# Performance work log

Measured on AMD Instinct MI355X. Metric: run time of the kernel, lower is better.

## Reference

```python
import jax, jax.numpy as jnp
import numpy as np
from jax import lax

B, L = 2, 1024
D_MODEL, D_STATE, EXPAND, D_CONV = 1024, 16, 2, 4
D_INNER = EXPAND * D_MODEL            # 2048
DT_RANK = (D_MODEL + 15) // 16        # 64


def setup_inputs() -> dict:
    key = jax.random.key(0)
    ks = jax.random.split(key, 8)
    g = lambda k, shape, s=0.02: jax.random.normal(k, shape, dtype=jnp.float32) * s
    # Mamba-style A init: A = -exp(A_log), A_log = log(1..d_state) per channel
    A_log = jnp.log(jnp.broadcast_to(
        jnp.arange(1, D_STATE + 1, dtype=jnp.float32), (D_INNER, D_STATE)))
    return {
        "x": jax.random.normal(ks[0], (B, L, D_MODEL), dtype=jnp.float32),
        "W_in": g(ks[1], (D_MODEL, 2 * D_INNER)),
        "conv_w": g(ks[2], (D_INNER, D_CONV), 0.1),
        "conv_b": jnp.zeros((D_INNER,), jnp.float32),
        "W_x": g(ks[3], (D_INNER, DT_RANK + 2 * D_STATE)),
        "W_dt": g(ks[4], (DT_RANK, D_INNER)),
        "b_dt": g(ks[5], (D_INNER,), 0.1),
        "A_log": A_log,
        "D_skip": jnp.ones((D_INNER,), jnp.float32),
        "W_out": g(ks[6], (D_INNER, D_MODEL)),
    }


def reference(x, W_in, conv_w, conv_b, W_x, W_dt, b_dt, A_log, D_skip, W_out):
    # in_proj -> (u, z): [B, L, D_INNER] each
    xz = x @ W_in
    u, z = xz[..., :D_INNER], xz[..., D_INNER:]

    # causal depthwise conv1d, kernel D_CONV (small fixed loop over taps)
    up = jnp.pad(u, ((0, 0), (D_CONV - 1, 0), (0, 0)))
    u = sum(up[:, k:k + L, :] * conv_w[:, k] for k in range(D_CONV)) + conv_b
    u = jax.nn.silu(u)

    # input-dependent dt, B, C
    x_dbl = u @ W_x                                    # [B, L, dt_rank + 2N]
    dt = x_dbl[..., :DT_RANK]
    Bm = x_dbl[..., DT_RANK:DT_RANK + D_STATE]         # [B, L, N]
    Cm = x_dbl[..., DT_RANK + D_STATE:]                # [B, L, N]
    delta = jax.nn.softplus(dt @ W_dt + b_dt)          # [B, L, D]

    A = -jnp.exp(A_log)                                # [D, N]
    deltaA = jnp.exp(jnp.einsum('bld,dn->bldn', delta, A))   # [B, L, D, N]
    dBu = (delta * u)[..., None] * Bm[:, :, None, :]          # [B, L, D, N]

    def step(h, inp):
        dA_t, dBu_t, c_t = inp                         # [B,D,N],[B,D,N],[B,N]
        h = dA_t * h + dBu_t
        y_t = jnp.einsum('bdn,bn->bd', h, c_t)
        return h, y_t

    h0 = jnp.zeros((B, D_INNER, D_STATE), x.dtype)
    _, ys = lax.scan(step, h0,
                     (deltaA.transpose(1, 0, 2, 3),
                      dBu.transpose(1, 0, 2, 3),
                      Cm.transpose(1, 0, 2)))
    y = ys.transpose(1, 0, 2) + u * D_skip             # [B, L, D_INNER]
    y = y * jax.nn.silu(z)                             # gated output
    return y @ W_out                                   # [B, L, D_MODEL]
```

## Files before the change

kernel.cpp:

```cpp
#include <hip/hip_runtime.h>


typedef unsigned short u16;
typedef unsigned int   u32;

#define B_SZ 2
#define L_SZ 1024
#define DM   1024
#define DI   2048
#define DS   16
#define DTR  64
#define NXD  96
#define NCHUNK 16
#define CL   64
#define KSPLIT 8
#define KC     256
#define OSPLIT 2

typedef __bf16 bf16x8 __attribute__((ext_vector_type(8)));
typedef float  f32x4  __attribute__((ext_vector_type(4)));

__device__ __forceinline__ u16 f2bf(float f) {
    u32 x = __float_as_uint(f);
    x += 0x7fffu + ((x >> 16) & 1u);
    return (u16)(x >> 16);
}
__device__ __forceinline__ float bf2f(u16 v) {
    return __uint_as_float(((u32)v) << 16);
}

__device__ __forceinline__ void gld_lds16(const u16* g, u16* l) {
    __builtin_amdgcn_global_load_lds(
        (const __attribute__((address_space(1))) u32*)g,
        (__attribute__((address_space(3))) u32*)l, 16, 0, 0);
}

__device__ __forceinline__ void wg_barrier() {
    __asm__ volatile("" ::: "memory");
    __builtin_amdgcn_s_barrier();
    __asm__ volatile("" ::: "memory");
}
#define WAIT_VM12() __builtin_amdgcn_s_waitcnt(0xF7C)
#define WAIT_VM8()  __builtin_amdgcn_s_waitcnt(0xF78)
#define WAIT_VM4()  __builtin_amdgcn_s_waitcnt(0xF74)
#define WAIT_VM0()  __builtin_amdgcn_s_waitcnt(0xF70)
#define WAIT_LGKM0() __builtin_amdgcn_s_waitcnt(0xC07F)

__global__ __launch_bounds__(256) void gemm128p(
    const u16* __restrict__ A, const u16* __restrict__ BT,
    float* __restrict__ Cf, u16* __restrict__ Cb,
    const float* __restrict__ bias,
    int M, int N, int K, int KCHUNK, int op)
{
    __shared__ u16 As[4][128 * 32];
    __shared__ u16 Bs[4][128 * 32];

    const int tid  = threadIdx.x;
    const int wave = tid >> 6;
    const int lane = tid & 63;
    const int q    = lane >> 4;
    const int r16  = lane & 15;
    const int wm   = (wave & 1) * 64;
    const int wn   = (wave >> 1) * 64;
    const int m0   = blockIdx.y * 128;
    const int n0   = blockIdx.x * 128;
    const int kb   = blockIdx.z * KCHUNK;

    const u16* gA0 = A  + (size_t)(m0 + (tid >> 2))      * K + (tid & 3) * 8;
    const u16* gA1 = A  + (size_t)(m0 + 64 + (tid >> 2)) * K + (tid & 3) * 8;
    const u16* gB0 = BT + (size_t)(n0 + (tid >> 2))      * K + (tid & 3) * 8;
    const u16* gB1 = BT + (size_t)(n0 + 64 + (tid >> 2)) * K + (tid & 3) * 8;

    const int niter = KCHUNK >> 5;

    const int pre = niter < 3 ? niter : 3;
    for (int p = 0; p < pre; ++p) {
        const int k0 = kb + p * 32;
        gld_lds16(gA0 + k0, &As[p][tid * 8]);
        gld_lds16(gA1 + k0, &As[p][2048 + tid * 8]);
        gld_lds16(gB0 + k0, &Bs[p][tid * 8]);
        gld_lds16(gB1 + k0, &Bs[p][2048 + tid * 8]);
    }

    f32x4 acc[4][4];
#pragma unroll
    for (int s = 0; s < 4; ++s)
#pragma unroll
        for (int j = 0; j < 4; ++j) acc[s][j] = (f32x4){0.f, 0.f, 0.f, 0.f};

    for (int it = 0; it < niter; ++it) {
        if (it + 3 < niter) {
            const int k0 = kb + (it + 3) * 32;
            const int bi = (it + 3) & 3;
            gld_lds16(gA0 + k0, &As[bi][tid * 8]);
            gld_lds16(gA1 + k0, &As[bi][2048 + tid * 8]);
            gld_lds16(gB0 + k0, &Bs[bi][tid * 8]);
            gld_lds16(gB1 + k0, &Bs[bi][2048 + tid * 8]);
            WAIT_VM12();
        } else if (it + 2 < niter) {
            WAIT_VM8();
        } else if (it + 1 < niter) {
            WAIT_VM4();
        } else {
            WAIT_VM0();
        }
        wg_barrier();

        const int cur = it & 3;
        bf16x8 af[4], bfr[4];
#pragma unroll
        for (int s = 0; s < 4; ++s)
            af[s] = *(const bf16x8*)(&As[cur][(wm + s * 16 + r16) * 32 + q * 8]);
#pragma unroll
        for (int j = 0; j < 4; ++j)
            bfr[j] = *(const bf16x8*)(&Bs[cur][(wn + j * 16 + r16) * 32 + q * 8]);
#pragma unroll
        for (int s = 0; s < 4; ++s)
#pragma unroll
            for (int j = 0; j < 4; ++j)
                acc[s][j] = __builtin_amdgcn_mfma_f32_16x16x32_bf16(
                    af[s], bfr[j], acc[s][j], 0, 0, 0);

        wg_barrier();
    }

#pragma unroll
    for (int s = 0; s < 4; ++s) {
        const int row0 = m0 + wm + s * 16 + q * 4;
#pragma unroll
        for (int j = 0; j < 4; ++j) {
            const int col = n0 + wn + j * 16 + r16;
            if (op == 0) {
                float* Cz = Cf + (size_t)blockIdx.z * M * N;
#pragma unroll
                for (int i = 0; i < 4; ++i)
                    Cz[(size_t)(row0 + i) * N + col] = acc[s][j][i];
            } else if (op == 1) {
                const float bv = bias[col];
#pragma unroll
                for (int i = 0; i < 4; ++i) {
                    float v = acc[s][j][i] + bv;
                    v = (v > 20.f) ? v : log1pf(__expf(v));
                    Cf[(size_t)(row0 + i) * N + col] = v;
                }
            } else {
#pragma unroll
                for (int i = 0; i < 4; ++i)
                    Cb[(size_t)(row0 + i) * N + col] = f2bf(acc[s][j][i]);
            }
        }
    }
}

__global__ __launch_bounds__(256) void reduce_out(
    const float* __restrict__ part, float* __restrict__ out, int n)
{
    const int i = (blockIdx.x * 256 + threadIdx.x) * 4;
    if (i >= n) return;
    f32x4 v = *(const f32x4*)(part + i);
#pragma unroll
    for (int s = 1; s < OSPLIT; ++s) {
        f32x4 p = *(const f32x4*)(part + (size_t)s * n + i);
        v.x += p.x; v.y += p.y; v.z += p.z; v.w += p.w;
    }
    *(f32x4*)(out + i) = v;
}

__global__ __launch_bounds__(256) void gemm_skinny_splitk(
    const u16* __restrict__ A, const u16* __restrict__ BT,
    float* __restrict__ Cpart, int M, int N, int K)
{
    constexpr int LDT = 40;
    __shared__ u16 As[128 * LDT];
    __shared__ u16 Bs[64 * LDT];

    const int tid  = threadIdx.x;
    const int wave = tid >> 6;
    const int lane = tid & 63;
    const int q    = lane >> 4;
    const int r16  = lane & 15;
    const int m0   = blockIdx.y * 128;
    const int n0   = blockIdx.x * 64;
    const int kcs  = blockIdx.z * KC;
    const int sr   = tid >> 2;
    const int ss   = (tid & 3) * 8;

    f32x4 acc[2][4];
#pragma unroll
    for (int s = 0; s < 2; ++s)
#pragma unroll
        for (int j = 0; j < 4; ++j) acc[s][j] = (f32x4){0.f, 0.f, 0.f, 0.f};

    const int bcol  = n0 + sr;
    const int bcolc = bcol < N ? bcol : N - 1;

    constexpr int NIT = KC / 32;
    uint4 a0 = *(const uint4*)(A + (size_t)(m0 + sr)      * K + kcs + ss);
    uint4 a1 = *(const uint4*)(A + (size_t)(m0 + 64 + sr) * K + kcs + ss);
    uint4 bv = *(const uint4*)(BT + (size_t)bcolc * K + kcs + ss);

    for (int it = 0; it < NIT; ++it) {
        wg_barrier();
        *(uint4*)(As + sr * LDT + ss)        = a0;
        *(uint4*)(As + (64 + sr) * LDT + ss) = a1;
        *(uint4*)(Bs + sr * LDT + ss)        = bv;
        const int kn = (it + 1 < NIT) ? (kcs + (it + 1) * 32) : kcs;
        a0 = *(const uint4*)(A + (size_t)(m0 + sr)      * K + kn + ss);
        a1 = *(const uint4*)(A + (size_t)(m0 + 64 + sr) * K + kn + ss);
        bv = *(const uint4*)(BT + (size_t)bcolc * K + kn + ss);
        WAIT_LGKM0();
        wg_barrier();

        bf16x8 af[2], bfr[4];
#pragma unroll
        for (int s = 0; s < 2; ++s)
            af[s] = *(const bf16x8*)(As + (wave * 32 + s * 16 + r16) * LDT + q * 8);
#pragma unroll
        for (int j = 0; j < 4; ++j)
            bfr[j] = *(const bf16x8*)(Bs + (j * 16 + r16) * LDT + q * 8);
#pragma unroll
        for (int s = 0; s < 2; ++s)
#pragma unroll
            for (int j = 0; j < 4; ++j)
                acc[s][j] = __builtin_amdgcn_mfma_f32_16x16x32_bf16(
                    af[s], bfr[j], acc[s][j], 0, 0, 0);
    }

    float* Cp = Cpart + (size_t)blockIdx.z * M * N;
#pragma unroll
    for (int s = 0; s < 2; ++s) {
        const int row0 = m0 + wave * 32 + s * 16 + q * 4;
#pragma unroll
        for (int j = 0; j < 4; ++j) {
            const int col = n0 + j * 16 + r16;
            if (col < N) {
#pragma unroll
                for (int i = 0; i < 4; ++i)
                    Cp[(size_t)(row0 + i) * N + col] = acc[s][j][i];
            }
        }
    }
}

__global__ __launch_bounds__(256) void reduce_xdbl(
    const float* __restrict__ part, float* __restrict__ xdbl,
    u16* __restrict__ dtbf)
{
    const int i = blockIdx.x * 256 + threadIdx.x;
    const int row = i / NXD, col = i - row * NXD;
    float v = 0.f;
#pragma unroll
    for (int s = 0; s < KSPLIT; ++s)
        v += part[(size_t)s * (B_SZ * L_SZ * NXD) + i];
    xdbl[i] = v;
    if (col < DTR) dtbf[row * DTR + col] = f2bf(v);
}

__device__ __forceinline__ void tr_tile(
    const float* __restrict__ in, u16* __restrict__ out,
    int R, int C, int tr, int tc, int tid, float (*t)[33])
{
    const int tx = tid & 31, ty = tid >> 5;
    const int r0 = tr * 32, c0 = tc * 32;
#pragma unroll
    for (int i = 0; i < 4; ++i) {
        int r = r0 + ty + i * 8, c = c0 + tx;
        if (r < R && c < C) t[ty + i * 8][tx] = in[(size_t)r * C + c];
    }
    __syncthreads();
#pragma unroll
    for (int i = 0; i < 4; ++i) {
        int oR = c0 + ty + i * 8, oC = r0 + tx;
        if (oR < C && oC < R) out[(size_t)oR * R + oC] = f2bf(t[tx][ty + i * 8]);
    }
}

__global__ __launch_bounds__(256) void prep_kernel(
    const float* __restrict__ x,     u16* __restrict__ xbf,
    const float* __restrict__ W_in,  u16* __restrict__ winT,
    const float* __restrict__ W_out, u16* __restrict__ woutT,
    const float* __restrict__ W_x,   u16* __restrict__ wxT,
    const float* __restrict__ W_dt,  u16* __restrict__ wdtT)
{
    __shared__ float t[32][33];
    const int id  = blockIdx.x;
    const int tid = threadIdx.x;
    if (id < 4096) {
        tr_tile(W_in, winT, 1024, 4096, id >> 7, id & 127, tid, t);
    } else if (id < 6144) {
        int i2 = id - 4096;
        tr_tile(W_out, woutT, 2048, 1024, i2 >> 5, i2 & 31, tid, t);
    } else if (id < 6336) {
        int i3 = id - 6144;
        tr_tile(W_x, wxT, 2048, 96, i3 / 3, i3 % 3, tid, t);
    } else if (id < 6464) {
        int i4 = id - 6336;
        tr_tile(W_dt, wdtT, 64, 2048, i4 >> 6, i4 & 63, tid, t);
    } else {
        int i = (id - 6464) * 256 + tid;
        xbf[i] = f2bf(x[i]);
    }
}

__global__ __launch_bounds__(256) void conv_silu_kernel(
    const u16* __restrict__ xzbf, const float* __restrict__ cw,
    const float* __restrict__ cb, u16* __restrict__ ucbf)
{
    const int idx = blockIdx.x * 256 + threadIdx.x;
    const int d   = idx & (DI - 1);
    const int pos = idx >> 11;
    const int l   = pos & (L_SZ - 1);
    float s = cb[d];
#pragma unroll
    for (int k = 0; k < 4; ++k) {
        int ls = l + k - 3;
        if (ls >= 0)
            s = fmaf(bf2f(xzbf[(size_t)(pos + k - 3) * (2 * DI) + d]), cw[d * 4 + k], s);
    }
    float v = s / (1.f + __expf(-s));
    ucbf[idx] = f2bf(v);
}

__global__ __launch_bounds__(256) void scan_pass1(
    const float* __restrict__ delta, const u16* __restrict__ ucbf,
    const float* __restrict__ xdbl, const float* __restrict__ A_log,
    float* __restrict__ hbuf, float* __restrict__ pbuf)
{
    const int c = blockIdx.x;
    const int d = blockIdx.y * 256 + threadIdx.x;
    const int b = blockIdx.z;
    float Av[16], h[16], P[16];
#pragma unroll
    for (int n = 0; n < 16; ++n) {
        Av[n] = -__expf(A_log[d * 16 + n]);
        h[n] = 0.f; P[n] = 1.f;
    }
    const int rowbase = b * L_SZ + c * CL;
    for (int i = 0; i < CL; ++i) {
        const int row = rowbase + i;
        float dlt = delta[(size_t)row * DI + d];
        float uu  = bf2f(ucbf[(size_t)row * DI + d]);
        float du  = dlt * uu;
        const float* xr = xdbl + (size_t)row * NXD;
#pragma unroll
        for (int n = 0; n < 16; ++n) {
            float e = __expf(dlt * Av[n]);
            P[n] *= e;
            h[n] = fmaf(e, h[n], du * xr[DTR + n]);
        }
    }
    size_t base = ((size_t)((b * NCHUNK + c) * DI + d)) * 16;
#pragma unroll
    for (int n = 0; n < 16; ++n) { hbuf[base + n] = h[n]; pbuf[base + n] = P[n]; }
}

__global__ __launch_bounds__(256) void scan_pass2(
    float* __restrict__ hbuf, const float* __restrict__ pbuf)
{
    const int j = blockIdx.x * 256 + threadIdx.x;
    const int b = blockIdx.y;
    float h0 = 0.f;
    for (int cc = 0; cc < NCHUNK; ++cc) {
        size_t o = ((size_t)(b * NCHUNK + cc)) * (DI * 16) + j;
        float hl = hbuf[o];
        float Pl = pbuf[o];
        hbuf[o] = h0;
        h0 = fmaf(Pl, h0, hl);
    }
}

__global__ __launch_bounds__(256) void scan_pass3(
    const float* __restrict__ delta, const u16* __restrict__ ucbf,
    const float* __restrict__ xdbl, const float* __restrict__ A_log,
    const float* __restrict__ hbuf, const u16* __restrict__ xzbf,
    const float* __restrict__ Dskip, u16* __restrict__ ybf)
{
    const int c = blockIdx.x;
    const int d = blockIdx.y * 256 + threadIdx.x;
    const int b = blockIdx.z;
    float Av[16], h[16];
    size_t base = ((size_t)((b * NCHUNK + c) * DI + d)) * 16;
#pragma unroll
    for (int n = 0; n < 16; ++n) {
        Av[n] = -__expf(A_log[d * 16 + n]);
        h[n]  = hbuf[base + n];
    }
    const float Dk = Dskip[d];
    const int rowbase = b * L_SZ + c * CL;
    for (int i = 0; i < CL; ++i) {
        const int row = rowbase + i;
        float dlt = delta[(size_t)row * DI + d];
        float uu  = bf2f(ucbf[(size_t)row * DI + d]);
        float du  = dlt * uu;
        const float* xr = xdbl + (size_t)row * NXD;
        float y = 0.f;
#pragma unroll
        for (int n = 0; n < 16; ++n) {
            float e = __expf(dlt * Av[n]);
            h[n] = fmaf(e, h[n], du * xr[DTR + n]);
            y = fmaf(h[n], xr[DTR + DS + n], y);
        }
        float zz = bf2f(xzbf[(size_t)row * (2 * DI) + DI + d]);
        float yv = fmaf(uu, Dk, y) * (zz / (1.f + __expf(-zz)));
        ybf[(size_t)row * DI + d] = f2bf(yv);
    }
}

constexpr size_t OFF_DELTA   = 0;
constexpr size_t OFF_XDBL    = OFF_DELTA + 4194304;
constexpr size_t OFF_SCRATCH = OFF_XDBL  + 196608;
constexpr size_t OFF_F32_END = OFF_SCRATCH + 8388608;
constexpr size_t SOFF_XBF   = 0;
constexpr size_t SOFF_WINT  = SOFF_XBF   + 2097152;
constexpr size_t SOFF_XZBF  = SOFF_WINT  + 4194304;
constexpr size_t SOFF_UCBF  = SOFF_XZBF  + 8388608;
constexpr size_t SOFF_WXT   = SOFF_UCBF  + 4194304;
constexpr size_t SOFF_DTBF  = SOFF_WXT   + 196608;
constexpr size_t SOFF_WDTT  = SOFF_DTBF  + 131072;
constexpr size_t SOFF_WOUTT = SOFF_WDTT  + 131072;
constexpr size_t SOFF_YBF   = SOFF_WOUTT + 2097152;

extern "C" void kernel_launch(void* const* d_in, const int* in_sizes, int n_in,
                              void* d_out, int out_size, void* d_ws, size_t ws_size,
                              hipStream_t stream)
{
    const float* x     = (const float*)d_in[0];
    const float* W_in  = (const float*)d_in[1];
    const float* cw    = (const float*)d_in[2];
    const float* cb    = (const float*)d_in[3];
    const float* W_x   = (const float*)d_in[4];
    const float* W_dt  = (const float*)d_in[5];
    const float* b_dt  = (const float*)d_in[6];
    const float* A_log = (const float*)d_in[7];
    const float* Dsk   = (const float*)d_in[8];
    const float* W_out = (const float*)d_in[9];
    float* out = (float*)d_out;

    float* wsf   = (float*)d_ws;
    float* dlt   = wsf + OFF_DELTA;
    float* xdbl  = wsf + OFF_XDBL;
    float* xpart = wsf + OFF_SCRATCH;
    float* hbuf  = wsf + OFF_SCRATCH;
    float* pbuf  = wsf + OFF_SCRATCH + 1048576;
    float* opart = wsf + OFF_SCRATCH;
    u16* sb    = (u16*)(wsf + OFF_F32_END);
    u16* xbf   = sb + SOFF_XBF;
    u16* winT  = sb + SOFF_WINT;
    u16* xzbf  = sb + SOFF_XZBF;
    u16* ucbf  = sb + SOFF_UCBF;
    u16* wxT   = sb + SOFF_WXT;
    u16* dtbf  = sb + SOFF_DTBF;
    u16* wdtT  = sb + SOFF_WDTT;
    u16* woutT = sb + SOFF_WOUTT;
    u16* ybf   = sb + SOFF_YBF;

    prep_kernel<<<14656, 256, 0, stream>>>(x, xbf, W_in, winT, W_out, woutT,
                                           W_x, wxT, W_dt, wdtT);

    gemm128p<<<dim3(32, 16, 1), 256, 0, stream>>>(
        xbf, winT, nullptr, xzbf, nullptr, 2048, 4096, 1024, 1024, 2);

    conv_silu_kernel<<<(B_SZ * L_SZ * DI) / 256, 256, 0, stream>>>(xzbf, cw, cb, ucbf);

    gemm_skinny_splitk<<<dim3(2, 16, KSPLIT), 256, 0, stream>>>(
        ucbf, wxT, xpart, 2048, NXD, 2048);
    reduce_xdbl<<<(B_SZ * L_SZ * NXD) / 256, 256, 0, stream>>>(xpart, xdbl, dtbf);

    gemm128p<<<dim3(16, 16, 1), 256, 0, stream>>>(
        dtbf, wdtT, dlt, nullptr, b_dt, 2048, 2048, 64, 64, 1);

    scan_pass1<<<dim3(NCHUNK, DI / 256, B_SZ), 256, 0, stream>>>(dlt, ucbf, xdbl, A_log, hbuf, pbuf);
    scan_pass2<<<dim3(DI * 16 / 256, B_SZ), 256, 0, stream>>>(hbuf, pbuf);
    scan_pass3<<<dim3(NCHUNK, DI / 256, B_SZ), 256, 0, stream>>>(dlt, ucbf, xdbl, A_log, hbuf, xzbf, Dsk, ybf);

    gemm128p<<<dim3(8, 16, OSPLIT), 256, 0, stream>>>(
        ybf, woutT, opart, nullptr, nullptr, 2048, 1024, 2048, 2048 / OSPLIT, 0);
    reduce_out<<<(2048 * 1024 / 4 + 255) / 256, 256, 0, stream>>>(
        opart, out, 2048 * 1024);
}
```

Before: 284.2 us.

## Drop split-K reduce kernels, use atomics for x_dbl, fuse dt cast into delta GEMM

```diff
diff --git a/kernel.cpp b/kernel.cpp
--- a/kernel.cpp
+++ b/kernel.cpp
@@ -11,11 +11,10 @@
 #define DS   16
 #define DTR  64
 #define NXD  96
-#define NCHUNK 16
-#define CL   64
+#define NCHUNK 32
+#define CL   32
 #define KSPLIT 8
 #define KC     256
-#define OSPLIT 2
 
 typedef __bf16 bf16x8 __attribute__((ext_vector_type(8)));
 typedef float  f32x4  __attribute__((ext_vector_type(4)));
@@ -41,16 +40,17 @@
     __asm__ volatile("" ::: "memory");
 }
 #define WAIT_VM12() __builtin_amdgcn_s_waitcnt(0xF7C)
+#define WAIT_VM9()  __builtin_amdgcn_s_waitcnt(0xF79)
 #define WAIT_VM8()  __builtin_amdgcn_s_waitcnt(0xF78)
+#define WAIT_VM6()  __builtin_amdgcn_s_waitcnt(0xF76)
 #define WAIT_VM4()  __builtin_amdgcn_s_waitcnt(0xF74)
+#define WAIT_VM3()  __builtin_amdgcn_s_waitcnt(0xF73)
 #define WAIT_VM0()  __builtin_amdgcn_s_waitcnt(0xF70)
-#define WAIT_LGKM0() __builtin_amdgcn_s_waitcnt(0xC07F)
 
 __global__ __launch_bounds__(256) void gemm128p(
     const u16* __restrict__ A, const u16* __restrict__ BT,
     float* __restrict__ Cf, u16* __restrict__ Cb,
-    const float* __restrict__ bias,
-    int M, int N, int K, int KCHUNK, int op)
+    int M, int N, int K, int op)
 {
     __shared__ u16 As[4][128 * 32];
     __shared__ u16 Bs[4][128 * 32];
@@ -64,18 +64,16 @@
     const int wn   = (wave >> 1) * 64;
     const int m0   = blockIdx.y * 128;
     const int n0   = blockIdx.x * 128;
-    const int kb   = blockIdx.z * KCHUNK;
 
     const u16* gA0 = A  + (size_t)(m0 + (tid >> 2))      * K + (tid & 3) * 8;
     const u16* gA1 = A  + (size_t)(m0 + 64 + (tid >> 2)) * K + (tid & 3) * 8;
     const u16* gB0 = BT + (size_t)(n0 + (tid >> 2))      * K + (tid & 3) * 8;
     const u16* gB1 = BT + (size_t)(n0 + 64 + (tid >> 2)) * K + (tid & 3) * 8;
 
-    const int niter = KCHUNK >> 5;
-
+    const int niter = K >> 5;
     const int pre = niter < 3 ? niter : 3;
     for (int p = 0; p < pre; ++p) {
-        const int k0 = kb + p * 32;
+        const int k0 = p * 32;
         gld_lds16(gA0 + k0, &As[p][tid * 8]);
         gld_lds16(gA1 + k0, &As[p][2048 + tid * 8]);
         gld_lds16(gB0 + k0, &Bs[p][tid * 8]);
@@ -90,7 +88,7 @@
 
     for (int it = 0; it < niter; ++it) {
         if (it + 3 < niter) {
-            const int k0 = kb + (it + 3) * 32;
+            const int k0 = (it + 3) * 32;
             const int bi = (it + 3) & 3;
             gld_lds16(gA0 + k0, &As[bi][tid * 8]);
             gld_lds16(gA1 + k0, &As[bi][2048 + tid * 8]);
@@ -130,45 +128,106 @@
 #pragma unroll
         for (int j = 0; j < 4; ++j) {
             const int col = n0 + wn + j * 16 + r16;
-            if (op == 0) {
-                float* Cz = Cf + (size_t)blockIdx.z * M * N;
-#pragma unroll
-                for (int i = 0; i < 4; ++i)
-                    Cz[(size_t)(row0 + i) * N + col] = acc[s][j][i];
-            } else if (op == 1) {
-                const float bv = bias[col];
-#pragma unroll
-                for (int i = 0; i < 4; ++i) {
-                    float v = acc[s][j][i] + bv;
-                    v = (v > 20.f) ? v : log1pf(__expf(v));
-                    Cf[(size_t)(row0 + i) * N + col] = v;
-                }
-            } else {
+            if (op == 2) {
 #pragma unroll
                 for (int i = 0; i < 4; ++i)
                     Cb[(size_t)(row0 + i) * N + col] = f2bf(acc[s][j][i]);
+            } else {
+#pragma unroll
+                for (int i = 0; i < 4; ++i)
+                    Cf[(size_t)(row0 + i) * N + col] = acc[s][j][i];
             }
         }
     }
 }
 
-__global__ __launch_bounds__(256) void reduce_out(
-    const float* __restrict__ part, float* __restrict__ out, int n)
-{
-    const int i = (blockIdx.x * 256 + threadIdx.x) * 4;
-    if (i >= n) return;
-    f32x4 v = *(const f32x4*)(part + i);
-#pragma unroll
-    for (int s = 1; s < OSPLIT; ++s) {
-        f32x4 p = *(const f32x4*)(part + (size_t)s * n + i);
-        v.x += p.x; v.y += p.y; v.z += p.z; v.w += p.w;
-    }
-    *(f32x4*)(out + i) = v;
-}
-
-__global__ __launch_bounds__(256) void gemm_skinny_splitk(
+__global__ __launch_bounds__(256) void gemm_out64(
     const u16* __restrict__ A, const u16* __restrict__ BT,
-    float* __restrict__ Cpart, int M, int N, int K)
+    float* __restrict__ C, int M, int N, int K)
+{
+    __shared__ u16 As[4][128 * 32];
+    __shared__ u16 Bs[4][64 * 32];
+
+    const int tid  = threadIdx.x;
+    const int wave = tid >> 6;
+    const int lane = tid & 63;
+    const int q    = lane >> 4;
+    const int r16  = lane & 15;
+    const int wm   = (wave & 1) * 64;
+    const int wn   = (wave >> 1) * 32;
+    const int m0   = blockIdx.y * 128;
+    const int n0   = blockIdx.x * 64;
+
+    const u16* gA0 = A  + (size_t)(m0 + (tid >> 2))      * K + (tid & 3) * 8;
+    const u16* gA1 = A  + (size_t)(m0 + 64 + (tid >> 2)) * K + (tid & 3) * 8;
+    const u16* gB0 = BT + (size_t)(n0 + (tid >> 2))      * K + (tid & 3) * 8;
+
+    const int niter = K >> 5;
+    const int pre = niter < 3 ? niter : 3;
+    for (int p = 0; p < pre; ++p) {
+        const int k0 = p * 32;
+        gld_lds16(gA0 + k0, &As[p][tid * 8]);
+        gld_lds16(gA1 + k0, &As[p][2048 + tid * 8]);
+        gld_lds16(gB0 + k0, &Bs[p][tid * 8]);
+    }
+
+    f32x4 acc[4][2];
+#pragma unroll
+    for (int s = 0; s < 4; ++s)
+#pragma unroll
+        for (int j = 0; j < 2; ++j) acc[s][j] = (f32x4){0.f, 0.f, 0.f, 0.f};
+
+    for (int it = 0; it < niter; ++it) {
+        if (it + 3 < niter) {
+            const int k0 = (it + 3) * 32;
+            const int bi = (it + 3) & 3;
+            gld_lds16(gA0 + k0, &As[bi][tid * 8]);
+            gld_lds16(gA1 + k0, &As[bi][2048 + tid * 8]);
+            gld_lds16(gB0 + k0, &Bs[bi][tid * 8]);
+            WAIT_VM9();
+        } else if (it + 2 < niter) {
+            WAIT_VM6();
+        } else if (it + 1 < niter) {
+            WAIT_VM3();
+        } else {
+            WAIT_VM0();
+        }
+        wg_barrier();
+
+        const int cur = it & 3;
+        bf16x8 af[4], bfr[2];
+#pragma unroll
+        for (int s = 0; s < 4; ++s)
+            af[s] = *(const bf16x8*)(&As[cur][(wm + s * 16 + r16) * 32 + q * 8]);
+#pragma unroll
+        for (int j = 0; j < 2; ++j)
+            bfr[j] = *(const bf16x8*)(&Bs[cur][(wn + j * 16 + r16) * 32 + q * 8]);
+#pragma unroll
+        for (int s = 0; s < 4; ++s)
+#pragma unroll
+            for (int j = 0; j < 2; ++j)
+                acc[s][j] = __builtin_amdgcn_mfma_f32_16x16x32_bf16(
+                    af[s], bfr[j], acc[s][j], 0, 0, 0);
+
+        wg_barrier();
+    }
+
+#pragma unroll
+    for (int s = 0; s < 4; ++s) {
+        const int row0 = m0 + wm + s * 16 + q * 4;
+#pragma unroll
+        for (int j = 0; j < 2; ++j) {
+            const int col = n0 + wn + j * 16 + r16;
+#pragma unroll
+            for (int i = 0; i < 4; ++i)
+                C[(size_t)(row0 + i) * N + col] = acc[s][j][i];
+        }
+    }
+}
+
+__global__ __launch_bounds__(256) void gemm_skinny_atomic(
+    const u16* __restrict__ A, const u16* __restrict__ BT,
+    float* xdbl, int M, int N, int K)
 {
     constexpr int LDT = 40;
     __shared__ u16 As[128 * LDT];
@@ -208,7 +267,8 @@
         a0 = *(const uint4*)(A + (size_t)(m0 + sr)      * K + kn + ss);
         a1 = *(const uint4*)(A + (size_t)(m0 + 64 + sr) * K + kn + ss);
         bv = *(const uint4*)(BT + (size_t)bcolc * K + kn + ss);
-        WAIT_LGKM0();
+        __builtin_amdgcn_s_waitcnt(0xF70 | 0x0000);
+        __builtin_amdgcn_s_waitcnt(0x070F);
         wg_barrier();
 
         bf16x8 af[2], bfr[4];
@@ -226,7 +286,6 @@
                     af[s], bfr[j], acc[s][j], 0, 0, 0);
     }
 
-    float* Cp = Cpart + (size_t)blockIdx.z * M * N;
 #pragma unroll
     for (int s = 0; s < 2; ++s) {
         const int row0 = m0 + wave * 32 + s * 16 + q * 4;
@@ -236,24 +295,86 @@
             if (col < N) {
 #pragma unroll
                 for (int i = 0; i < 4; ++i)
-                    Cp[(size_t)(row0 + i) * N + col] = acc[s][j][i];
+                    atomicAdd(&xdbl[(size_t)(row0 + i) * N + col], acc[s][j][i]);
             }
         }
     }
 }
 
-__global__ __launch_bounds__(256) void reduce_xdbl(
-    const float* __restrict__ part, float* __restrict__ xdbl,
-    u16* __restrict__ dtbf)
-{
-    const int i = blockIdx.x * 256 + threadIdx.x;
-    const int row = i / NXD, col = i - row * NXD;
-    float v = 0.f;
-#pragma unroll
-    for (int s = 0; s < KSPLIT; ++s)
-        v += part[(size_t)s * (B_SZ * L_SZ * NXD) + i];
-    xdbl[i] = v;
-    if (col < DTR) dtbf[row * DTR + col] = f2bf(v);
+__global__ __launch_bounds__(256) void gemm_delta(
+    const float* __restrict__ xdbl, const u16* __restrict__ BT,
+    const float* __restrict__ bias, float* __restrict__ dlt)
+{
+    constexpr int LDT = 40;
+    __shared__ u16 As[128 * LDT];
+    __shared__ u16 Bs[128 * LDT];
+
+    const int tid  = threadIdx.x;
+    const int wave = tid >> 6;
+    const int lane = tid & 63;
+    const int q    = lane >> 4;
+    const int r16  = lane & 15;
+    const int wm   = (wave & 1) * 64;
+    const int wn   = (wave >> 1) * 64;
+    const int m0   = blockIdx.y * 128;
+    const int n0   = blockIdx.x * 128;
+    const int sr   = tid >> 2;
+    const int ss   = (tid & 3) * 8;
+
+    f32x4 acc[4][4];
+#pragma unroll
+    for (int s = 0; s < 4; ++s)
+#pragma unroll
+        for (int j = 0; j < 4; ++j) acc[s][j] = (f32x4){0.f, 0.f, 0.f, 0.f};
+
+    for (int k0 = 0; k0 < DTR; k0 += 32) {
+        __syncthreads();
+        f32x4 f0 = *(const f32x4*)(xdbl + (size_t)(m0 + sr) * NXD + k0 + ss);
+        f32x4 f1 = *(const f32x4*)(xdbl + (size_t)(m0 + sr) * NXD + k0 + ss + 4);
+        f32x4 f2 = *(const f32x4*)(xdbl + (size_t)(m0 + 64 + sr) * NXD + k0 + ss);
+        f32x4 f3 = *(const f32x4*)(xdbl + (size_t)(m0 + 64 + sr) * NXD + k0 + ss + 4);
+        uint4 bv0 = *(const uint4*)(BT + (size_t)(n0 + sr)      * DTR + k0 + ss);
+        uint4 bv1 = *(const uint4*)(BT + (size_t)(n0 + 64 + sr) * DTR + k0 + ss);
+        u16* pa0 = As + sr * LDT + ss;
+        u16* pa1 = As + (64 + sr) * LDT + ss;
+#pragma unroll
+        for (int i = 0; i < 4; ++i) { pa0[i] = f2bf(f0[i]); pa0[4 + i] = f2bf(f1[i]); }
+#pragma unroll
+        for (int i = 0; i < 4; ++i) { pa1[i] = f2bf(f2[i]); pa1[4 + i] = f2bf(f3[i]); }
+        *(uint4*)(Bs + sr * LDT + ss)        = bv0;
+        *(uint4*)(Bs + (64 + sr) * LDT + ss) = bv1;
+        __syncthreads();
+
+        bf16x8 af[4], bfr[4];
+#pragma unroll
+        for (int s = 0; s < 4; ++s)
+            af[s] = *(const bf16x8*)(As + (wm + s * 16 + r16) * LDT + q * 8);
+#pragma unroll
+        for (int j = 0; j < 4; ++j)
+            bfr[j] = *(const bf16x8*)(Bs + (wn + j * 16 + r16) * LDT + q * 8);
+#pragma unroll
+        for (int s = 0; s < 4; ++s)
+#pragma unroll
+            for (int j = 0; j < 4; ++j)
+                acc[s][j] = __builtin_amdgcn_mfma_f32_16x16x32_bf16(
+                    af[s], bfr[j], acc[s][j], 0, 0, 0);
+    }
+
+#pragma unroll
+    for (int s = 0; s < 4; ++s) {
+        const int row0 = m0 + wm + s * 16 + q * 4;
+#pragma unroll
+        for (int j = 0; j < 4; ++j) {
+            const int col = n0 + wn + j * 16 + r16;
+            const float bv = bias[col];
+#pragma unroll
+            for (int i = 0; i < 4; ++i) {
+                float v = acc[s][j][i] + bv;
+                v = (v > 20.f) ? v : log1pf(__expf(v));
+                dlt[(size_t)(row0 + i) * DI + col] = v;
+            }
+        }
+    }
 }
 
 __device__ __forceinline__ void tr_tile(
@@ -280,7 +401,8 @@
     const float* __restrict__ W_in,  u16* __restrict__ winT,
     const float* __restrict__ W_out, u16* __restrict__ woutT,
     const float* __restrict__ W_x,   u16* __restrict__ wxT,
-    const float* __restrict__ W_dt,  u16* __restrict__ wdtT)
+    const float* __restrict__ W_dt,  u16* __restrict__ wdtT,
+    float* __restrict__ xdbl)
 {
     __shared__ float t[32][33];
     const int id  = blockIdx.x;
@@ -296,9 +418,12 @@
     } else if (id < 6464) {
         int i4 = id - 6336;
         tr_tile(W_dt, wdtT, 64, 2048, i4 >> 6, i4 & 63, tid, t);
-    } else {
+    } else if (id < 14656) {
         int i = (id - 6464) * 256 + tid;
         xbf[i] = f2bf(x[i]);
+    } else {
+        f32x4 z = (f32x4){0.f, 0.f, 0.f, 0.f};
+        ((f32x4*)xdbl)[(size_t)(id - 14656) * 256 + tid] = z;
     }
 }
 
@@ -408,15 +533,15 @@
 
 constexpr size_t OFF_DELTA   = 0;
 constexpr size_t OFF_XDBL    = OFF_DELTA + 4194304;
-constexpr size_t OFF_SCRATCH = OFF_XDBL  + 196608;
-constexpr size_t OFF_F32_END = OFF_SCRATCH + 8388608;
+constexpr size_t OFF_HBUF    = OFF_XDBL  + 196608;
+constexpr size_t OFF_PBUF    = OFF_HBUF  + 2097152;
+constexpr size_t OFF_F32_END = OFF_PBUF  + 2097152;
 constexpr size_t SOFF_XBF   = 0;
 constexpr size_t SOFF_WINT  = SOFF_XBF   + 2097152;
 constexpr size_t SOFF_XZBF  = SOFF_WINT  + 4194304;
 constexpr size_t SOFF_UCBF  = SOFF_XZBF  + 8388608;
 constexpr size_t SOFF_WXT   = SOFF_UCBF  + 4194304;
-constexpr size_t SOFF_DTBF  = SOFF_WXT   + 196608;
-constexpr size_t SOFF_WDTT  = SOFF_DTBF  + 131072;
+constexpr size_t SOFF_WDTT  = SOFF_WXT   + 196608;
 constexpr size_t SOFF_WOUTT = SOFF_WDTT  + 131072;
 constexpr size_t SOFF_YBF   = SOFF_WOUTT + 2097152;
 
@@ -439,42 +564,34 @@
     float* wsf   = (float*)d_ws;
     float* dlt   = wsf + OFF_DELTA;
     float* xdbl  = wsf + OFF_XDBL;
-    float* xpart = wsf + OFF_SCRATCH;
-    float* hbuf  = wsf + OFF_SCRATCH;
-    float* pbuf  = wsf + OFF_SCRATCH + 1048576;
-    float* opart = wsf + OFF_SCRATCH;
+    float* hbuf  = wsf + OFF_HBUF;
+    float* pbuf  = wsf + OFF_PBUF;
     u16* sb    = (u16*)(wsf + OFF_F32_END);
     u16* xbf   = sb + SOFF_XBF;
     u16* winT  = sb + SOFF_WINT;
     u16* xzbf  = sb + SOFF_XZBF;
     u16* ucbf  = sb + SOFF_UCBF;
     u16* wxT   = sb + SOFF_WXT;
-    u16* dtbf  = sb + SOFF_DTBF;
     u16* wdtT  = sb + SOFF_WDTT;
     u16* woutT = sb + SOFF_WOUTT;
     u16* ybf   = sb + SOFF_YBF;
 
-    prep_kernel<<<14656, 256, 0, stream>>>(x, xbf, W_in, winT, W_out, woutT,
-                                           W_x, wxT, W_dt, wdtT);
-
-    gemm128p<<<dim3(32, 16, 1), 256, 0, stream>>>(
-        xbf, winT, nullptr, xzbf, nullptr, 2048, 4096, 1024, 1024, 2);
+    prep_kernel<<<14848, 256, 0, stream>>>(x, xbf, W_in, winT, W_out, woutT,
+                                           W_x, wxT, W_dt, wdtT, xdbl);
+
+    gemm128p<<<dim3(32, 16), 256, 0, stream>>>(
+        xbf, winT, nullptr, xzbf, 2048, 4096, 1024, 2);
 
     conv_silu_kernel<<<(B_SZ * L_SZ * DI) / 256, 256, 0, stream>>>(xzbf, cw, cb, ucbf);
 
-    gemm_skinny_splitk<<<dim3(2, 16, KSPLIT), 256, 0, stream>>>(
-        ucbf, wxT, xpart, 2048, NXD, 2048);
-    reduce_xdbl<<<(B_SZ * L_SZ * NXD) / 256, 256, 0, stream>>>(xpart, xdbl, dtbf);
-
-    gemm128p<<<dim3(16, 16, 1), 256, 0, stream>>>(
-        dtbf, wdtT, dlt, nullptr, b_dt, 2048, 2048, 64, 64, 1);
+    gemm_skinny_atomic<<<dim3(2, 16, KSPLIT), 256, 0, stream>>>(
+        ucbf, wxT, xdbl, 2048, NXD, 2048);
+
+    gemm_delta<<<dim3(16, 16), 256, 0, stream>>>(xdbl, wdtT, b_dt, dlt);
 
     scan_pass1<<<dim3(NCHUNK, DI / 256, B_SZ), 256, 0, stream>>>(dlt, ucbf, xdbl, A_log, hbuf, pbuf);
     scan_pass2<<<dim3(DI * 16 / 256, B_SZ), 256, 0, stream>>>(hbuf, pbuf);
     scan_pass3<<<dim3(NCHUNK, DI / 256, B_SZ), 256, 0, stream>>>(dlt, ucbf, xdbl, A_log, hbuf, xzbf, Dsk, ybf);
 
-    gemm128p<<<dim3(8, 16, OSPLIT), 256, 0, stream>>>(
-        ybf, woutT, opart, nullptr, nullptr, 2048, 1024, 2048, 2048 / OSPLIT, 0);
-    reduce_out<<<(2048 * 1024 / 4 + 255) / 256, 256, 0, stream>>>(
-        opart, out, 2048 * 1024);
-}
+    gemm_out64<<<dim3(16, 16), 256, 0, stream>>>(ybf, woutT, out, 2048, 1024, 2048);
+}
```

Result: faster. 262.9 us (-7.5%).
